# Optimization experiments

Measured on AMD Instinct MI355X. Metric: run time of the kernel, lower is better.

The kernel has to match this reference:

```python
import jax, jax.numpy as jnp
import numpy as np

LEVEL = 3
NUM_BANDS = LEVEL + 1
B, N, D_MODEL, PATCH_NUMS, PRED_LEN = 32, 7, 768, 64, 336

# db4 lowpass decomposition filter (pywt convention)
_DB4_DEC_LO = np.array([
    -0.010597401784997278, 0.032883011666982945, 0.030841381835986965,
    -0.18703481171888114, -0.02798376941698385, 0.6308807679295904,
    0.7148465705525415, 0.23037781330885523], dtype=np.float32)
REC_LO = _DB4_DEC_LO[::-1].copy()                                   # reconstruction lowpass
REC_HI = (_DB4_DEC_LO * ((-1.0) ** (np.arange(8) + 1))).astype(np.float32)  # reconstruction highpass (QMF)


def _upsample2(x):
    # zero-interleave along last axis: (..., L) -> (..., 2L)
    z = jnp.zeros_like(x)
    return jnp.stack([x, z], axis=-1).reshape(*x.shape[:-1], 2 * x.shape[-1])


def _idwt_per(ca, cd, rec_lo, rec_hi):
    # single-level inverse DWT, periodization mode, along last axis: (..., L) -> (..., 2L)
    F = rec_lo.shape[0]
    ua, ud = _upsample2(ca), _upsample2(cd)
    y = jnp.zeros_like(ua)
    for k in range(F):  # small fixed tap loop (F=8)
        y = y + jnp.roll(ua, k, axis=-1) * rec_lo[k] + jnp.roll(ud, k, axis=-1) * rec_hi[k]
    return jnp.roll(y, -(F // 2 - 1), axis=-1)  # compensate filter delay


def _iswt(coeffs, level, rec_lo, rec_hi):
    # coeffs: (..., T, level+1) with bands ordered [cA, cD_level, ..., cD1]
    T = coeffs.shape[-2]
    out = coeffs[..., 0]
    for j in range(level, 0, -1):
        step = 2 ** (j - 1)
        cd = coeffs[..., level - j + 1]
        M = T // step
        # gather the `step` interleaved subsequences as a batch axis: (..., step, M)
        o = jnp.moveaxis(out.reshape(*out.shape[:-1], M, step), -1, -2)
        d = jnp.moveaxis(cd.reshape(*cd.shape[:-1], M, step), -1, -2)
        x1 = _idwt_per(o[..., 0::2], d[..., 0::2], rec_lo, rec_hi)
        x2 = jnp.roll(_idwt_per(o[..., 1::2], d[..., 1::2], rec_lo, rec_hi), 1, axis=-1)
        new = 0.5 * (x1 + x2)  # (..., step, M)
        out = jnp.moveaxis(new, -2, -1).reshape(*out.shape[:-1], T)
    return out


def setup_inputs() -> dict:
    key = jax.random.key(0)
    kx, kw, kb = jax.random.split(key, 3)
    Din = D_MODEL * PATCH_NUMS
    x = jax.random.normal(kx, (B, N, D_MODEL, PATCH_NUMS), dtype=jnp.float32)
    # Linear init ~ U(-1/sqrt(Din), 1/sqrt(Din)); small normal is equivalent for a reference
    W = jax.random.normal(kw, (NUM_BANDS, Din, PRED_LEN), dtype=jnp.float32) * (1.0 / np.sqrt(Din))
    b = jax.random.normal(kb, (NUM_BANDS, PRED_LEN), dtype=jnp.float32) * 0.01
    return {"x": x, "W": W, "b": b}


def reference(x, W, b):
    # x: (B, N, d_model, patch_nums); W: (bands, d_model*patch_nums, pred_len); b: (bands, pred_len)
    Bb, Nn, dm, P = x.shape
    xf = x.reshape(Bb, Nn, dm * P)  # Flatten(start_dim=-2)
    # all band projections as one batched GEMM -> (B, N, pred_len, bands)
    coeffs = jnp.einsum('bnd,kdp->bnpk', xf, W) + b.T
    rec_lo = jnp.asarray(REC_LO)
    rec_hi = jnp.asarray(REC_HI)
    return _iswt(coeffs, LEVEL, rec_lo, rec_hi)  # (B, N, pred_len)
```

## Files before the change

kernel.cpp:

```cpp
#include <hip/hip_runtime.h>
#include <stdint.h>

#define M_ROWS   224
#define K_DIM    49152
#define NCOL     1344
#define PRED     336
#define S_CHUNKS 48
#define STEPS    32

#define XB_OFFSET (32u * 1024u * 1024u)

typedef __attribute__((ext_vector_type(8))) short short8;
typedef __attribute__((ext_vector_type(4))) float floatx4;

__device__ __forceinline__ uint16_t f32_to_bf16(float f) {
    uint32_t u = __builtin_bit_cast(uint32_t, f);
    uint32_t r = (u + 0x7fffu + ((u >> 16) & 1u)) >> 16;
    return (uint16_t)r;
}
__device__ __forceinline__ float bf16_to_f32(uint16_t h) {
    uint32_t u = ((uint32_t)h) << 16;
    return __builtin_bit_cast(float, u);
}
__device__ __forceinline__ uint32_t pack2(float lo, float hi) {
    return (uint32_t)f32_to_bf16(lo) | ((uint32_t)f32_to_bf16(hi) << 16);
}

__global__ __launch_bounds__(256) void cvt_x(
    const float* __restrict__ X, uint16_t* __restrict__ Xb)
{
    const size_t i = ((size_t)blockIdx.x * 256 + threadIdx.x) * 8;
    const float4 a = *(const float4*)(X + i);
    const float4 b = *(const float4*)(X + i + 4);
    uint4 o;
    o.x = pack2(a.x, a.y);
    o.y = pack2(a.z, a.w);
    o.z = pack2(b.x, b.y);
    o.w = pack2(b.z, b.w);
    *(uint4*)(Xb + i) = o;
}

__global__ __launch_bounds__(256, 3) void gemm_partial(
    const uint16_t* __restrict__ Xb,
    const float* __restrict__ W,
    uint16_t* __restrict__ P)
{
    __shared__ uint16_t lX[3][14 * 512];

    const int id = blockIdx.x;
    const int g  = id & 7;
    const int q  = id >> 3;
    const int ct = q % 21;
    const int s  = g + 8 * (q / 21);

    const int tid  = threadIdx.x;
    const int lane = tid & 63;
    const int w    = tid >> 6;
    const int l15  = lane & 15;
    const int kq   = lane >> 4;
    const int c0w  = ct * 64 + w * 16;
    const int band = c0w / PRED;
    const int p0   = c0w - band * PRED;

    const float* wbase = W + (size_t)band * ((size_t)K_DIM * PRED)
                           + (size_t)(kq * 8) * PRED
                           + (size_t)(p0 + l15);
    const size_t grow = (size_t)l15 * K_DIM + (size_t)kq * 8;
    const int kbase = s * (STEPS * 32);

    floatx4 acc[14];
    #pragma unroll
    for (int f = 0; f < 14; ++f) acc[f] = (floatx4){0.f, 0.f, 0.f, 0.f};

    float wA[8], wB[8];

    #pragma unroll
    for (int b = 0; b < 2; ++b) {
        #pragma unroll
        for (int t = 0; t < 4; ++t) {
            const int f = w + 4 * t;
            if (f < 14) {
                const uint16_t* gp = Xb + (size_t)(16 * f) * K_DIM + grow
                                        + kbase + b * 32;
                __builtin_amdgcn_global_load_lds(
                    (const __attribute__((address_space(1))) void*)gp,
                    (__attribute__((address_space(3))) void*)&lX[b][f * 512],
                    16, 0, 0);
            }
        }
    }
    #pragma unroll
    for (int j = 0; j < 8; ++j) wA[j] = wbase[(size_t)(kbase + j) * PRED];
    #pragma unroll
    for (int j = 0; j < 8; ++j) wB[j] = wbase[(size_t)(kbase + 32 + j) * PRED];
    asm volatile("s_waitcnt vmcnt(0)" ::: "memory");
    __builtin_amdgcn_s_barrier();
    __builtin_amdgcn_sched_barrier(0);

#define GEMM_STEP(ST, XR, XW, WREG, DO_PRE, WAITSTR)                           \
    {                                                                          \
        if (DO_PRE) {                                                          \
            const int kx = kbase + ((ST) + 2) * 32;                            \
            _Pragma("unroll")                                                  \
            for (int t = 0; t < 4; ++t) {                                      \
                const int f = w + 4 * t;                                       \
                if (f < 14) {                                                  \
                    const uint16_t* gp = Xb + (size_t)(16*f)*K_DIM + grow + kx;\
                    __builtin_amdgcn_global_load_lds(                          \
                        (const __attribute__((address_space(1))) void*)gp,     \
                        (__attribute__((address_space(3))) void*)&lX[XW][f*512],\
                        16, 0, 0);                                             \
                }                                                              \
            }                                                                  \
        }                                                                      \
        short8 bfrag;                                                          \
        _Pragma("unroll")                                                      \
        for (int j = 0; j < 4; ++j)                                            \
            ((uint32_t*)&bfrag)[j] = pack2(WREG[2*j], WREG[2*j+1]);            \
        if (DO_PRE) {                                                          \
            const int kw2 = kbase + ((ST) + 2) * 32;                           \
            _Pragma("unroll")                                                  \
            for (int j = 0; j < 8; ++j)                                        \
                WREG[j] = wbase[(size_t)(kw2 + j) * PRED];                     \
        }                                                                      \
        _Pragma("unroll")                                                      \
        for (int f = 0; f < 14; ++f) {                                         \
            short8 afrag = *(const short8*)&lX[XR][f * 512 + lane * 8];        \
            acc[f] = __builtin_amdgcn_mfma_f32_16x16x32_bf16(                  \
                afrag, bfrag, acc[f], 0, 0, 0);                                \
        }                                                                      \
        asm volatile("s_waitcnt " WAITSTR " lgkmcnt(0)" ::: "memory");         \
        __builtin_amdgcn_s_barrier();                                          \
        __builtin_amdgcn_sched_barrier(0);                                     \
    }

    for (int st = 0; st < 30; st += 6) {
        GEMM_STEP(st + 0, 0, 2, wA, 1, "vmcnt(11)")
        GEMM_STEP(st + 1, 1, 0, wB, 1, "vmcnt(11)")
        GEMM_STEP(st + 2, 2, 1, wA, 1, "vmcnt(11)")
        GEMM_STEP(st + 3, 0, 2, wB, 1, "vmcnt(11)")
        GEMM_STEP(st + 4, 1, 0, wA, 1, "vmcnt(11)")
        GEMM_STEP(st + 5, 2, 1, wB, 1, "vmcnt(11)")
    }
    GEMM_STEP(30, 0, 2, wA, 0, "vmcnt(0)")
    GEMM_STEP(31, 1, 0, wB, 0, "vmcnt(0)")
#undef GEMM_STEP

    const int col = c0w + l15;
    #pragma unroll
    for (int f = 0; f < 14; ++f) {
        #pragma unroll
        for (int r = 0; r < 4; ++r) {
            const int m = 16 * f + kq * 4 + r;
            P[((size_t)m * S_CHUNKS + s) * NCOL + col] = f32_to_bf16(acc[f][r]);
        }
    }
}

__device__ const float REC_LO[8] = {
     0.23037781330885523f,  0.7148465705525415f,   0.6308807679295904f,
    -0.02798376941698385f, -0.18703481171888114f,  0.030841381835986965f,
     0.032883011666982945f, -0.010597401784997278f };
__device__ const float REC_HI[8] = {
     0.010597401784997278f, 0.032883011666982945f, -0.030841381835986965f,
    -0.18703481171888114f,  0.02798376941698385f,   0.6308807679295904f,
    -0.7148465705525415f,   0.23037781330885523f };

__global__ __launch_bounds__(1024) void reduce_iswt(
    const uint16_t* __restrict__ P,
    const float* __restrict__ bias,
    float* __restrict__ out)
{
    __shared__ float coeff[NCOL];
    __shared__ float buf[2][PRED];

    const int row = blockIdx.x;
    const int tid = threadIdx.x;
    const uint32_t* pr = (const uint32_t*)(P + (size_t)row * S_CHUNKS * NCOL);

    if (tid < NCOL / 2) {
        float a0 = 0.f, a1 = 0.f;
        #pragma unroll 8
        for (int s = 0; s < S_CHUNKS; ++s) {
            const uint32_t v = pr[s * (NCOL / 2) + tid];
            a0 += bf16_to_f32((uint16_t)(v & 0xffff));
            a1 += bf16_to_f32((uint16_t)(v >> 16));
        }
        coeff[2 * tid]     = a0 + bias[2 * tid];
        coeff[2 * tid + 1] = a1 + bias[2 * tid + 1];
    }
    __syncthreads();

    if (tid < PRED) buf[0][tid] = coeff[tid];
    __syncthreads();

    int curb = 0;
    for (int j = 3; j >= 1; --j) {
        const int step = 1 << (j - 1);
        const int M    = PRED / step;
        const float* cd  = &coeff[(4 - j) * PRED];
        const float* cur = buf[curb];
        float* nxt       = buf[curb ^ 1];
        if (tid < PRED) {
            const int t = tid;
            const int sidx = t & (step - 1);
            const int m = t / step;
            const int mm1 = (m == 0) ? (M - 1) : (m - 1);
            float x1 = 0.f, x2 = 0.f;
            #pragma unroll
            for (int k = 0; k < 8; ++k) {
                int i1 = m + 3 - k;  if (i1 < 0) i1 += M; else if (i1 >= M) i1 -= M;
                if ((i1 & 1) == 0) {
                    const int pos = i1 * step + sidx;
                    x1 += cur[pos] * REC_LO[k] + cd[pos] * REC_HI[k];
                }
                int i2 = mm1 + 3 - k;  if (i2 < 0) i2 += M; else if (i2 >= M) i2 -= M;
                if ((i2 & 1) == 0) {
                    const int pos = (i2 + 1) * step + sidx;
                    x2 += cur[pos] * REC_LO[k] + cd[pos] * REC_HI[k];
                }
            }
            nxt[t] = 0.5f * (x1 + x2);
        }
        __syncthreads();
        curb ^= 1;
    }

    if (tid < PRED) out[(size_t)row * PRED + tid] = buf[curb][tid];
}

extern "C" void kernel_launch(void* const* d_in, const int* in_sizes, int n_in,
                              void* d_out, int out_size, void* d_ws, size_t ws_size,
                              hipStream_t stream) {
    const float* X    = (const float*)d_in[0];
    const float* W    = (const float*)d_in[1];
    const float* bias = (const float*)d_in[2];
    float* out        = (float*)d_out;
    uint16_t* P       = (uint16_t*)d_ws;
    uint16_t* Xb      = (uint16_t*)((char*)d_ws + XB_OFFSET);

    cvt_x       <<<5376, 256, 0, stream>>>(X, Xb);
    gemm_partial<<<21 * S_CHUNKS, 256, 0, stream>>>(Xb, W, P);
    reduce_iswt <<<M_ROWS, 1024, 0, stream>>>(P, bias, out);
}
```

Before: 428.4 us.

## Widen GEMM column tile per wave to reuse X fragments across two B tiles

Each wave now computes two 16-column output tiles, so every X fragment read from LDS feeds two MFMAs and the block covers 96 columns with 3 waves instead of 64 with 4. Block count drops from 21 to 14 column tiles per K chunk, which cuts repeated loading of X into LDS across column tiles. The cost is double the accumulator registers (occupancy hint lowered to 2), fewer total blocks, and the vmcnt wait counts were retuned for the extra loads in flight.

```diff
diff --git a/kernel.cpp b/kernel.cpp
--- a/kernel.cpp
+++ b/kernel.cpp
@@ -7,6 +7,7 @@
 #define PRED     336
 #define S_CHUNKS 48
 #define STEPS    32
+#define CTILES   14
 
 #define XB_OFFSET (32u * 1024u * 1024u)
 
@@ -40,7 +41,7 @@
     *(uint4*)(Xb + i) = o;
 }
 
-__global__ __launch_bounds__(256, 3) void gemm_partial(
+__global__ __launch_bounds__(192, 2) void gemm_partial(
     const uint16_t* __restrict__ Xb,
     const float* __restrict__ W,
     uint16_t* __restrict__ P)
@@ -50,35 +51,42 @@
     const int id = blockIdx.x;
     const int g  = id & 7;
     const int q  = id >> 3;
-    const int ct = q % 21;
-    const int s  = g + 8 * (q / 21);
+    const int ct = q % CTILES;
+    const int s  = g + 8 * (q / CTILES);
 
     const int tid  = threadIdx.x;
     const int lane = tid & 63;
     const int w    = tid >> 6;
     const int l15  = lane & 15;
     const int kq   = lane >> 4;
-    const int c0w  = ct * 64 + w * 16;
-    const int band = c0w / PRED;
-    const int p0   = c0w - band * PRED;
-
-    const float* wbase = W + (size_t)band * ((size_t)K_DIM * PRED)
-                           + (size_t)(kq * 8) * PRED
-                           + (size_t)(p0 + l15);
+
+    const int c0w   = ct * 96 + w * 32;
+    const int c1w   = c0w + 16;
+    const int band0 = c0w / PRED, band1 = c1w / PRED;
+    const int p00   = c0w - band0 * PRED;
+    const int p01   = c1w - band1 * PRED;
+
+    const float* wbase0 = W + (size_t)band0 * ((size_t)K_DIM * PRED)
+                            + (size_t)(kq * 8) * PRED + (size_t)(p00 + l15);
+    const float* wbase1 = W + (size_t)band1 * ((size_t)K_DIM * PRED)
+                            + (size_t)(kq * 8) * PRED + (size_t)(p01 + l15);
     const size_t grow = (size_t)l15 * K_DIM + (size_t)kq * 8;
     const int kbase = s * (STEPS * 32);
 
-    floatx4 acc[14];
-    #pragma unroll
-    for (int f = 0; f < 14; ++f) acc[f] = (floatx4){0.f, 0.f, 0.f, 0.f};
-
-    float wA[8], wB[8];
+    floatx4 acc0[14], acc1[14];
+    #pragma unroll
+    for (int f = 0; f < 14; ++f) {
+        acc0[f] = (floatx4){0.f, 0.f, 0.f, 0.f};
+        acc1[f] = (floatx4){0.f, 0.f, 0.f, 0.f};
+    }
+
+    float wA0[8], wA1[8], wB0[8], wB1[8];
 
     #pragma unroll
     for (int b = 0; b < 2; ++b) {
         #pragma unroll
-        for (int t = 0; t < 4; ++t) {
-            const int f = w + 4 * t;
+        for (int t = 0; t < 5; ++t) {
+            const int f = w + 3 * t;
             if (f < 14) {
                 const uint16_t* gp = Xb + (size_t)(16 * f) * K_DIM + grow
                                         + kbase + b * 32;
@@ -90,20 +98,26 @@
         }
     }
     #pragma unroll
-    for (int j = 0; j < 8; ++j) wA[j] = wbase[(size_t)(kbase + j) * PRED];
-    #pragma unroll
-    for (int j = 0; j < 8; ++j) wB[j] = wbase[(size_t)(kbase + 32 + j) * PRED];
+    for (int j = 0; j < 8; ++j) {
+        wA0[j] = wbase0[(size_t)(kbase + j) * PRED];
+        wA1[j] = wbase1[(size_t)(kbase + j) * PRED];
+    }
+    #pragma unroll
+    for (int j = 0; j < 8; ++j) {
+        wB0[j] = wbase0[(size_t)(kbase + 32 + j) * PRED];
+        wB1[j] = wbase1[(size_t)(kbase + 32 + j) * PRED];
+    }
     asm volatile("s_waitcnt vmcnt(0)" ::: "memory");
     __builtin_amdgcn_s_barrier();
     __builtin_amdgcn_sched_barrier(0);
 
-#define GEMM_STEP(ST, XR, XW, WREG, DO_PRE, WAITSTR)                           \
+#define GEMM_STEP(ST, XR, XW, WR0, WR1, DO_PRE, WAITSTR)                       \
     {                                                                          \
         if (DO_PRE) {                                                          \
             const int kx = kbase + ((ST) + 2) * 32;                            \
             _Pragma("unroll")                                                  \
-            for (int t = 0; t < 4; ++t) {                                      \
-                const int f = w + 4 * t;                                       \
+            for (int t = 0; t < 5; ++t) {                                      \
+                const int f = w + 3 * t;                                       \
                 if (f < 14) {                                                  \
                     const uint16_t* gp = Xb + (size_t)(16*f)*K_DIM + grow + kx;\
                     __builtin_amdgcn_global_load_lds(                          \
@@ -113,21 +127,27 @@
                 }                                                              \
             }                                                                  \
         }                                                                      \
-        short8 bfrag;                                                          \
+        short8 bfrag0, bfrag1;                                                 \
         _Pragma("unroll")                                                      \
-        for (int j = 0; j < 4; ++j)                                            \
-            ((uint32_t*)&bfrag)[j] = pack2(WREG[2*j], WREG[2*j+1]);            \
+        for (int j = 0; j < 4; ++j) {                                          \
+            ((uint32_t*)&bfrag0)[j] = pack2(WR0[2*j], WR0[2*j+1]);             \
+            ((uint32_t*)&bfrag1)[j] = pack2(WR1[2*j], WR1[2*j+1]);             \
+        }                                                                      \
         if (DO_PRE) {                                                          \
             const int kw2 = kbase + ((ST) + 2) * 32;                           \
             _Pragma("unroll")                                                  \
-            for (int j = 0; j < 8; ++j)                                        \
-                WREG[j] = wbase[(size_t)(kw2 + j) * PRED];                     \
+            for (int j = 0; j < 8; ++j) {                                      \
+                WR0[j] = wbase0[(size_t)(kw2 + j) * PRED];                     \
+                WR1[j] = wbase1[(size_t)(kw2 + j) * PRED];                     \
+            }                                                                  \
         }                                                                      \
         _Pragma("unroll")                                                      \
         for (int f = 0; f < 14; ++f) {                                         \
             short8 afrag = *(const short8*)&lX[XR][f * 512 + lane * 8];        \
-            acc[f] = __builtin_amdgcn_mfma_f32_16x16x32_bf16(                  \
-                afrag, bfrag, acc[f], 0, 0, 0);                                \
+            acc0[f] = __builtin_amdgcn_mfma_f32_16x16x32_bf16(                 \
+                afrag, bfrag0, acc0[f], 0, 0, 0);                              \
+            acc1[f] = __builtin_amdgcn_mfma_f32_16x16x32_bf16(                 \
+                afrag, bfrag1, acc1[f], 0, 0, 0);                              \
         }                                                                      \
         asm volatile("s_waitcnt " WAITSTR " lgkmcnt(0)" ::: "memory");         \
         __builtin_amdgcn_s_barrier();                                          \
@@ -135,24 +155,27 @@
     }
 
     for (int st = 0; st < 30; st += 6) {
-        GEMM_STEP(st + 0, 0, 2, wA, 1, "vmcnt(11)")
-        GEMM_STEP(st + 1, 1, 0, wB, 1, "vmcnt(11)")
-        GEMM_STEP(st + 2, 2, 1, wA, 1, "vmcnt(11)")
-        GEMM_STEP(st + 3, 0, 2, wB, 1, "vmcnt(11)")
-        GEMM_STEP(st + 4, 1, 0, wA, 1, "vmcnt(11)")
-        GEMM_STEP(st + 5, 2, 1, wB, 1, "vmcnt(11)")
-    }
-    GEMM_STEP(30, 0, 2, wA, 0, "vmcnt(0)")
-    GEMM_STEP(31, 1, 0, wB, 0, "vmcnt(0)")
+        GEMM_STEP(st + 0, 0, 2, wA0, wA1, 1, "vmcnt(20)")
+        GEMM_STEP(st + 1, 1, 0, wB0, wB1, 1, "vmcnt(20)")
+        GEMM_STEP(st + 2, 2, 1, wA0, wA1, 1, "vmcnt(20)")
+        GEMM_STEP(st + 3, 0, 2, wB0, wB1, 1, "vmcnt(20)")
+        GEMM_STEP(st + 4, 1, 0, wA0, wA1, 1, "vmcnt(20)")
+        GEMM_STEP(st + 5, 2, 1, wB0, wB1, 1, "vmcnt(20)")
+    }
+    GEMM_STEP(30, 0, 2, wA0, wA1, 0, "vmcnt(0)")
+    GEMM_STEP(31, 1, 0, wB0, wB1, 0, "vmcnt(0)")
 #undef GEMM_STEP
 
-    const int col = c0w + l15;
+    const int col0 = c0w + l15;
+    const int col1 = c1w + l15;
     #pragma unroll
     for (int f = 0; f < 14; ++f) {
         #pragma unroll
         for (int r = 0; r < 4; ++r) {
             const int m = 16 * f + kq * 4 + r;
-            P[((size_t)m * S_CHUNKS + s) * NCOL + col] = f32_to_bf16(acc[f][r]);
+            const size_t base = ((size_t)m * S_CHUNKS + s) * NCOL;
+            P[base + col0] = f32_to_bf16(acc0[f][r]);
+            P[base + col1] = f32_to_bf16(acc1[f][r]);
         }
     }
 }
@@ -240,6 +263,6 @@
     uint16_t* Xb      = (uint16_t*)((char*)d_ws + XB_OFFSET);
 
     cvt_x       <<<5376, 256, 0, stream>>>(X, Xb);
-    gemm_partial<<<21 * S_CHUNKS, 256, 0, stream>>>(Xb, W, P);
+    gemm_partial<<<CTILES * S_CHUNKS, 192, 0, stream>>>(Xb, W, P);
     reduce_iswt <<<M_ROWS, 1024, 0, stream>>>(P, bias, out);
 }
```

New measurement: 425.7 us. Within noise of the previous version (-0.6%).
